# Kernel optimization log

Hardware: AMD Instinct MI355X
Metric: run time of the kernel (lower is better)

The kernel has to match this reference:

```python
import jax, jax.numpy as jnp
import numpy as np

N_NODES = 8192
N_EDGES = 262144
IN_DIM = 256
HID = 256
OUT_DIM = 64
PATH_DIM = 64
N_HEADS = 4


def setup_inputs() -> dict:
    key = jax.random.key(0)
    ks = jax.random.split(key, 16)
    s = 0.05
    x = jax.random.normal(ks[0], (N_NODES, IN_DIM), dtype=jnp.float32)
    edge_index = jax.random.randint(ks[1], (2, N_EDGES), 0, N_NODES, dtype=jnp.int32)
    return {
        "x": x,
        "edge_index": edge_index,
        # pathway encoder Linear(IN_DIM, PATH_DIM)
        "pe_w": jax.random.normal(ks[2], (IN_DIM, PATH_DIM), jnp.float32) * s,
        "pe_b": jax.random.normal(ks[3], (PATH_DIM,), jnp.float32) * s,
        # MultiheadAttention packed in-proj [3E, E] and out-proj [E, E]
        "in_proj_w": jax.random.normal(ks[4], (3 * PATH_DIM, PATH_DIM), jnp.float32) * s,
        "in_proj_b": jax.random.normal(ks[5], (3 * PATH_DIM,), jnp.float32) * s,
        "out_proj_w": jax.random.normal(ks[6], (PATH_DIM, PATH_DIM), jnp.float32) * s,
        "out_proj_b": jax.random.normal(ks[7], (PATH_DIM,), jnp.float32) * s,
        # GCN layer weights (in_dim, out_dim) + bias
        "w1": jax.random.normal(ks[8], (IN_DIM + PATH_DIM, HID), jnp.float32) * s,
        "b1": jax.random.normal(ks[9], (HID,), jnp.float32) * s,
        "w2": jax.random.normal(ks[10], (HID, HID), jnp.float32) * s,
        "b2": jax.random.normal(ks[11], (HID,), jnp.float32) * s,
        "w3": jax.random.normal(ks[12], (HID, OUT_DIM), jnp.float32) * s,
        "b3": jax.random.normal(ks[13], (OUT_DIM,), jnp.float32) * s,
    }


def mha_self(x, in_proj_w, in_proj_b, out_proj_w, out_proj_b):
    # unbatched nn.MultiheadAttention: x [N, E], Q=K=V=x
    N, E = x.shape
    dh = E // N_HEADS
    qkv = x @ in_proj_w.T + in_proj_b  # [N, 3E]
    q, k, v = jnp.split(qkv, 3, axis=-1)
    # [H, N, dh]
    q = q.reshape(N, N_HEADS, dh).transpose(1, 0, 2)
    k = k.reshape(N, N_HEADS, dh).transpose(1, 0, 2)
    v = v.reshape(N, N_HEADS, dh).transpose(1, 0, 2)
    scores = jnp.einsum('hnd,hmd->hnm', q, k) / jnp.sqrt(jnp.float32(dh))
    attn = jax.nn.softmax(scores, axis=-1)
    out = jnp.einsum('hnm,hmd->hnd', attn, v)  # [H, N, dh]
    out = out.transpose(1, 0, 2).reshape(N, E)
    return out @ out_proj_w.T + out_proj_b


def gcn_conv(h, edge_index, w, b, num_nodes):
    # PyG GCNConv: add self loops, symmetric normalization, linear, scatter-add, bias
    src = jnp.concatenate([edge_index[0], jnp.arange(num_nodes, dtype=edge_index.dtype)])
    dst = jnp.concatenate([edge_index[1], jnp.arange(num_nodes, dtype=edge_index.dtype)])
    deg = jax.ops.segment_sum(jnp.ones_like(dst, dtype=h.dtype), dst, num_segments=num_nodes)
    dinv = jnp.where(deg > 0, jax.lax.rsqrt(jnp.maximum(deg, 1e-12)), 0.0)
    hw = h @ w  # [N, out]
    norm = (dinv[src] * dinv[dst])[:, None]
    msg = hw[src] * norm
    out = jax.ops.segment_sum(msg, dst, num_segments=num_nodes)
    return out + b


def reference(x, edge_index, pe_w, pe_b, in_proj_w, in_proj_b, out_proj_w, out_proj_b,
              w1, b1, w2, b2, w3, b3):
    N = x.shape[0]
    pf = x @ pe_w + pe_b  # pathway encoder
    pa = mha_self(pf, in_proj_w, in_proj_b, out_proj_w, out_proj_b)
    h = jnp.concatenate([x, pa], axis=-1)  # [N, IN_DIM + PATH_DIM]
    h = jax.nn.relu(gcn_conv(h, edge_index, w1, b1, N))  # dropout is identity (eval)
    h = jax.nn.relu(gcn_conv(h, edge_index, w2, b2, N))
    h = gcn_conv(h, edge_index, w3, b3, N)
    return h
```

## Files before the change

kernel.cpp:

```cpp
#include <hip/hip_runtime.h>
#include <hip/hip_bf16.h>

#define N_NODES 8192
#define N_EDGES 262144
#define IN_DIM 256
#define HID 256
#define OUT_DIM 64
#define PATH_DIM 64
#define NHEADS 4
#define DH 16
#define KSPLIT 8
#define SPLIT_KEYS (N_NODES / KSPLIT)
#define NCHUNK (SPLIT_KEYS / 64)

typedef __attribute__((ext_vector_type(8))) short bf16x8;
typedef __attribute__((ext_vector_type(4))) float f32x4;

__device__ __forceinline__ ushort f2bf(float f) {
  union { float f; unsigned int u; } c;
  c.f = f;
  unsigned int u = c.u;
  u += 0x7fffu + ((u >> 16) & 1u);
  return (ushort)(u >> 16);
}

__device__ __forceinline__ float fast_exp2(float x) {
  float r;
  asm("v_exp_f32 %0, %1" : "=v"(r) : "v"(x));
  return r;
}

__device__ __forceinline__ unsigned pack_bf16(float a, float b) {
  union { __hip_bfloat162 h; unsigned u; } c;
  c.h = __float22bfloat162_rn(make_float2(a, b));
  return c.u;
}


__global__ __launch_bounds__(256) void init_graph(int* deg, int* cursor) {
  int i = blockIdx.x * 256 + threadIdx.x;
  if (i < N_NODES) { deg[i] = 1; cursor[i] = 0; }
}

__global__ __launch_bounds__(256) void count_deg(const int* __restrict__ dst,
                                                 int* __restrict__ deg) {
  int e = blockIdx.x * 256 + threadIdx.x;
  if (e < N_EDGES) atomicAdd(&deg[dst[e]], 1);
}

__global__ __launch_bounds__(256) void scan_rows(const int* __restrict__ deg,
                                                 int* __restrict__ row_off,
                                                 float* __restrict__ dinv) {
  __shared__ int part[256];
  int t = threadIdx.x;
  int base = t * 32;
  int local[32];
  int s = 0;
  #pragma unroll
  for (int i = 0; i < 32; ++i) {
    int c = deg[base + i] - 1;
    local[i] = s;
    s += c;
  }
  part[t] = s;
  __syncthreads();
  for (int d = 1; d < 256; d <<= 1) {
    int v = (t >= d) ? part[t - d] : 0;
    __syncthreads();
    part[t] += v;
    __syncthreads();
  }
  int prev = (t == 0) ? 0 : part[t - 1];
  #pragma unroll
  for (int i = 0; i < 32; ++i) {
    row_off[base + i] = prev + local[i];
    dinv[base + i] = rsqrtf((float)deg[base + i]);
  }
}

__global__ __launch_bounds__(256) void fill_csr(const int* __restrict__ src,
                                                const int* __restrict__ dst,
                                                const int* __restrict__ row_off,
                                                int* __restrict__ cursor,
                                                int* __restrict__ csr) {
  int e = blockIdx.x * 256 + threadIdx.x;
  if (e < N_EDGES) {
    int d = dst[e];
    int p = atomicAdd(&cursor[d], 1);
    csr[row_off[d] + p] = src[e];
  }
}


__global__ __launch_bounds__(256) void transpose_w(const float* __restrict__ W,
                                                   float* __restrict__ Wt,
                                                   int R, int C) {
  int i = blockIdx.x * 256 + threadIdx.x;
  if (i < R * C) {
    int r = i / C, c = i % C;
    Wt[c * R + r] = W[i];
  }
}

__global__ __launch_bounds__(256) void convert_qkv(const float* __restrict__ qkv,
                                                   ushort* __restrict__ Qbf,
                                                   ushort* __restrict__ Kbf,
                                                   ushort* __restrict__ Vtb) {
  const int tg = blockIdx.x * 256 + threadIdx.x;
  const int h = tg >> 13;
  const int n = tg & 8191;
  const float SC = 0.36067376022224085f;
  const float* base = qkv + (size_t)n * 192 + h * 16;
  ushort* qd = Qbf + ((size_t)h * 8192 + n) * 32;
  ushort* kd = Kbf + ((size_t)h * 8192 + n) * 32;
  ushort4 zz = make_ushort4(0, 0, 0, 0);
  #pragma unroll
  for (int i = 0; i < 16; i += 4) {
    float4 q4 = *reinterpret_cast<const float4*>(base + i);
    float4 k4 = *reinterpret_cast<const float4*>(base + 64 + i);
    float4 v4 = *reinterpret_cast<const float4*>(base + 128 + i);
    *reinterpret_cast<ushort4*>(qd + i) =
        make_ushort4(f2bf(q4.x * SC), f2bf(q4.y * SC), f2bf(q4.z * SC), f2bf(q4.w * SC));
    *reinterpret_cast<ushort4*>(kd + i) =
        make_ushort4(f2bf(k4.x), f2bf(k4.y), f2bf(k4.z), f2bf(k4.w));
    *reinterpret_cast<ushort4*>(qd + 16 + i) = zz;
    *reinterpret_cast<ushort4*>(kd + 16 + i) = zz;
    Vtb[((size_t)h * 16 + i + 0) * 8192 + n] = f2bf(v4.x);
    Vtb[((size_t)h * 16 + i + 1) * 8192 + n] = f2bf(v4.y);
    Vtb[((size_t)h * 16 + i + 2) * 8192 + n] = f2bf(v4.z);
    Vtb[((size_t)h * 16 + i + 3) * 8192 + n] = f2bf(v4.w);
  }
}


template <bool RELU, bool BIAS>
__global__ __launch_bounds__(256) void gemm_tile(const float* __restrict__ A1, int K1,
                                                 const float* __restrict__ A2, int K2,
                                                 const float* __restrict__ B,
                                                 const float* __restrict__ bias,
                                                 float* __restrict__ C, int N) {
  __shared__ __align__(16) float As[16][64];
  __shared__ __align__(16) float Bs[16][68];
  const int K = K1 + K2;
  const int bm = blockIdx.y * 64;
  const int bn = blockIdx.x * 64;
  const int t = threadIdx.x;
  const int tx = t & 15, ty = t >> 4;
  const int am = t >> 2;
  const int ak = (t & 3) << 2;
  const int bk = t >> 4;
  const int bn4 = (t & 15) << 2;
  float acc[4][4] = {};
  for (int k0 = 0; k0 < K; k0 += 16) {
    int kk = k0 + ak;
    int row = bm + am;
    float4 av;
    if (kk < K1)
      av = *reinterpret_cast<const float4*>(A1 + (size_t)row * K1 + kk);
    else
      av = *reinterpret_cast<const float4*>(A2 + (size_t)row * K2 + (kk - K1));
    As[ak + 0][am] = av.x;
    As[ak + 1][am] = av.y;
    As[ak + 2][am] = av.z;
    As[ak + 3][am] = av.w;
    float4 bv = *reinterpret_cast<const float4*>(B + (size_t)(k0 + bk) * N + bn + bn4);
    *reinterpret_cast<float4*>(&Bs[bk][bn4]) = bv;
    __syncthreads();
    #pragma unroll
    for (int k = 0; k < 16; ++k) {
      float4 a = *reinterpret_cast<const float4*>(&As[k][ty << 2]);
      float4 b = *reinterpret_cast<const float4*>(&Bs[k][tx << 2]);
      acc[0][0] += a.x * b.x; acc[0][1] += a.x * b.y; acc[0][2] += a.x * b.z; acc[0][3] += a.x * b.w;
      acc[1][0] += a.y * b.x; acc[1][1] += a.y * b.y; acc[1][2] += a.y * b.z; acc[1][3] += a.y * b.w;
      acc[2][0] += a.z * b.x; acc[2][1] += a.z * b.y; acc[2][2] += a.z * b.z; acc[2][3] += a.z * b.w;
      acc[3][0] += a.w * b.x; acc[3][1] += a.w * b.y; acc[3][2] += a.w * b.z; acc[3][3] += a.w * b.w;
    }
    __syncthreads();
  }
  #pragma unroll
  for (int i = 0; i < 4; ++i) {
    int row = bm + (ty << 2) + i;
    float4 o = make_float4(acc[i][0], acc[i][1], acc[i][2], acc[i][3]);
    if (BIAS) {
      float4 bv = *reinterpret_cast<const float4*>(bias + bn + (tx << 2));
      o.x += bv.x; o.y += bv.y; o.z += bv.z; o.w += bv.w;
    }
    if (RELU) {
      o.x = fmaxf(o.x, 0.f); o.y = fmaxf(o.y, 0.f);
      o.z = fmaxf(o.z, 0.f); o.w = fmaxf(o.w, 0.f);
    }
    *reinterpret_cast<float4*>(C + (size_t)row * N + bn + (tx << 2)) = o;
  }
}


__global__ __launch_bounds__(256) void attn_mfma4(const ushort* __restrict__ Qbf,
                                                  const ushort* __restrict__ Kbf,
                                                  const ushort* __restrict__ Vtb,
                                                  float* __restrict__ Opart,
                                                  float* __restrict__ Wpart) {
  const int h  = blockIdx.y;
  const int qb = blockIdx.x;
  const int kz = blockIdx.z;
  const int t  = threadIdx.x;
  const int wv = t >> 6;
  const int l  = t & 63;
  const int lg = l >> 4;
  const int lc = l & 15;

  __shared__ __align__(16) ushort Ps[64][64];
  __shared__ __align__(16) ushort Vls[2][16][64];
  __shared__ float wred[4][64];

  bf16x8 qf[4];
  {
    const ushort* qbase = Qbf + ((size_t)h * 8192 + qb * 64) * 32;
    #pragma unroll
    for (int qt = 0; qt < 4; ++qt)
      qf[qt] = *reinterpret_cast<const bf16x8*>(qbase + (qt * 16 + lc) * 32 + lg * 8);
  }

  const ushort* kbase =
      Kbf + (size_t)h * 8192 * 32 + ((size_t)kz * SPLIT_KEYS + wv * 16 + lc) * 32 + lg * 8;

  const int vrow = t >> 4;
  const int vcol8 = t & 15;
  const ushort* vsrc = Vtb + ((size_t)h * 16 + vrow) * 8192 + kz * SPLIT_KEYS + vcol8 * 4;
  const int vdst = vrow * 128 + (((vcol8 >> 1) ^ (vrow & 7)) << 4) + (vcol8 & 1) * 8;

  const int pw_off = (((wv * 2 + (lg >> 1)) ^ (lc & 7)) << 4) + (lg & 1) * 8;
  int pr_off[2], vr_off[2];
  #pragma unroll
  for (int half = 0; half < 2; ++half) {
    int g = (half * 4 + lg) ^ (lc & 7);
    pr_off[half] = (wv * 16 + lc) * 128 + g * 16;
    vr_off[half] = lc * 128 + g * 16;
  }

  char* ps_base  = (char*)&Ps[0][0];
  char* vls_base = (char*)&Vls[0][0][0];

  *reinterpret_cast<ushort4*>(vls_base + vdst) =
      *reinterpret_cast<const ushort4*>(vsrc);
  bf16x8 kf = *reinterpret_cast<const bf16x8*>(kbase);

  f32x4 oacc = {0.f, 0.f, 0.f, 0.f};
  float wsumP[4] = {0.f, 0.f, 0.f, 0.f};

  __syncthreads();

  for (int c = 0; c < NCHUNK; ++c) {
    const bool more = (c + 1 < NCHUNK);
    ushort4 vpre;
    bf16x8 kf_n;
    if (more) {
      vpre = *reinterpret_cast<const ushort4*>(vsrc + (c + 1) * 64);
      kf_n = *reinterpret_cast<const bf16x8*>(kbase + (size_t)(c + 1) * 64 * 32);
    }

    f32x4 s[4];
    #pragma unroll
    for (int qt = 0; qt < 4; ++qt) {
      f32x4 z = {0.f, 0.f, 0.f, 0.f};
      s[qt] = __builtin_amdgcn_mfma_f32_16x16x32_bf16(kf, qf[qt], z, 0, 0, 0);
    }
    kf = kf_n;

    #pragma unroll
    for (int qt = 0; qt < 4; ++qt) {
      float e0 = fast_exp2(s[qt][0]);
      float e1 = fast_exp2(s[qt][1]);
      float e2 = fast_exp2(s[qt][2]);
      float e3 = fast_exp2(s[qt][3]);
      wsumP[qt] += (e0 + e1) + (e2 + e3);
      uint2 pk;
      pk.x = pack_bf16(e0, e1);
      pk.y = pack_bf16(e2, e3);
      *reinterpret_cast<uint2*>(ps_base + (qt * 16 + lc) * 128 + pw_off) = pk;
    }

    if (more)
      *reinterpret_cast<ushort4*>(vls_base + ((c + 1) & 1) * 2048 + vdst) = vpre;

    __syncthreads();

    char* vlb = vls_base + (c & 1) * 2048;
    #pragma unroll
    for (int half = 0; half < 2; ++half) {
      bf16x8 pf = *reinterpret_cast<const bf16x8*>(ps_base + pr_off[half]);
      bf16x8 vf = *reinterpret_cast<const bf16x8*>(vlb + vr_off[half]);
      oacc = __builtin_amdgcn_mfma_f32_16x16x32_bf16(pf, vf, oacc, 0, 0, 0);
    }

    __syncthreads();
  }

  #pragma unroll
  for (int qt = 0; qt < 4; ++qt) {
    float v = wsumP[qt];
    v += __shfl_xor(v, 16);
    v += __shfl_xor(v, 32);
    wsumP[qt] = v;
  }
  if (lg == 0) {
    #pragma unroll
    for (int qt = 0; qt < 4; ++qt) wred[wv][qt * 16 + lc] = wsumP[qt];
  }
  __syncthreads();

  const size_t obase = ((size_t)(kz * NHEADS + h) * N_NODES + qb * 64);
  #pragma unroll
  for (int r = 0; r < 4; ++r) {
    const int qrow = wv * 16 + lg * 4 + r;
    Opart[(obase + qrow) * 16 + lc] = oacc[r];
  }
  if (t < 64) {
    float ws = wred[0][t] + wred[1][t] + wred[2][t] + wred[3][t];
    Wpart[obase + t] = ws;
  }
}

__global__ __launch_bounds__(256) void attn_combine(const float* __restrict__ Opart,
                                                    const float* __restrict__ Wpart,
                                                    float* __restrict__ attn_out) {
  int i = blockIdx.x * 256 + threadIdx.x;
  int dq = i & 3;
  int hn = i >> 2;
  int h = hn >> 13;
  int n = hn & 8191;
  float4 acc = make_float4(0.f, 0.f, 0.f, 0.f);
  float ws = 0.f;
  #pragma unroll
  for (int s = 0; s < KSPLIT; ++s) {
    const size_t row = ((size_t)(s * NHEADS + h) * N_NODES + n);
    float4 v = *reinterpret_cast<const float4*>(Opart + row * 16 + dq * 4);
    acc.x += v.x; acc.y += v.y; acc.z += v.z; acc.w += v.w;
    ws += Wpart[row];
  }
  float inv = 1.f / ws;
  float4 o = make_float4(acc.x * inv, acc.y * inv, acc.z * inv, acc.w * inv);
  *reinterpret_cast<float4*>(attn_out + (size_t)n * 64 + h * 16 + dq * 4) = o;
}


template <bool RELU>
__global__ __launch_bounds__(256) void aggregate2(const float* __restrict__ hw,
                                                  const int* __restrict__ csr,
                                                  const int* __restrict__ row_off,
                                                  const int* __restrict__ deg,
                                                  const float* __restrict__ dinv,
                                                  const float* __restrict__ bias,
                                                  float* __restrict__ out) {
  __shared__ __align__(16) float part[2][256];
  const int t = threadIdx.x;
  const int rw = t >> 7;
  const int wh = (t >> 6) & 1;
  const int l = t & 63;
  const int r = blockIdx.x * 2 + rw;
  const float dr = dinv[r];
  const int off = row_off[r];
  const int cnt = deg[r] - 1;
  const int c = l << 2;

  float ax, ay, az, aw;
  if (wh == 0) {
    float4 a = *reinterpret_cast<const float4*>(hw + (size_t)r * 256 + c);
    ax = dr * a.x; ay = dr * a.y; az = dr * a.z; aw = dr * a.w;
  } else {
    ax = ay = az = aw = 0.f;
  }
  for (int e = wh; e < cnt; e += 2) {
    int s = csr[off + e];
    float wsc = dinv[s];
    float4 hv = *reinterpret_cast<const float4*>(hw + (size_t)s * 256 + c);
    ax += wsc * hv.x; ay += wsc * hv.y; az += wsc * hv.z; aw += wsc * hv.w;
  }
  if (wh == 1)
    *reinterpret_cast<float4*>(&part[rw][c]) = make_float4(ax, ay, az, aw);
  __syncthreads();
  if (wh == 0) {
    float4 p = *reinterpret_cast<const float4*>(&part[rw][c]);
    float4 bv = *reinterpret_cast<const float4*>(bias + c);
    float4 o;
    o.x = dr * (ax + p.x) + bv.x;
    o.y = dr * (ay + p.y) + bv.y;
    o.z = dr * (az + p.z) + bv.z;
    o.w = dr * (aw + p.w) + bv.w;
    if (RELU) {
      o.x = fmaxf(o.x, 0.f); o.y = fmaxf(o.y, 0.f);
      o.z = fmaxf(o.z, 0.f); o.w = fmaxf(o.w, 0.f);
    }
    *reinterpret_cast<float4*>(out + (size_t)r * 256 + c) = o;
  }
}

template <bool RELU>
__global__ __launch_bounds__(256) void aggregate64(const float* __restrict__ hw,
                                                   const int* __restrict__ csr,
                                                   const int* __restrict__ row_off,
                                                   const int* __restrict__ deg,
                                                   const float* __restrict__ dinv,
                                                   const float* __restrict__ bias,
                                                   float* __restrict__ out) {
  const int w = threadIdx.x >> 6, l = threadIdx.x & 63;
  const int r = blockIdx.x * 4 + w;
  const float dr = dinv[r];
  const int off = row_off[r];
  const int cnt = deg[r] - 1;
  float a = dr * hw[(size_t)r * 64 + l];
  for (int e = 0; e < cnt; ++e) {
    int s = csr[off + e];
    a += dinv[s] * hw[(size_t)s * 64 + l];
  }
  float o = dr * a + bias[l];
  if (RELU) o = fmaxf(o, 0.f);
  out[(size_t)r * 64 + l] = o;
}


extern "C" void kernel_launch(void* const* d_in, const int* in_sizes, int n_in,
                              void* d_out, int out_size, void* d_ws, size_t ws_size,
                              hipStream_t stream) {
  const float* x          = (const float*)d_in[0];
  const int*   ei         = (const int*)d_in[1];
  const float* pe_w       = (const float*)d_in[2];
  const float* pe_b       = (const float*)d_in[3];
  const float* in_proj_w  = (const float*)d_in[4];
  const float* in_proj_b  = (const float*)d_in[5];
  const float* out_proj_w = (const float*)d_in[6];
  const float* out_proj_b = (const float*)d_in[7];
  const float* w1         = (const float*)d_in[8];
  const float* b1         = (const float*)d_in[9];
  const float* w2         = (const float*)d_in[10];
  const float* b2         = (const float*)d_in[11];
  const float* w3         = (const float*)d_in[12];
  const float* b3         = (const float*)d_in[13];

  const int* esrc = ei;
  const int* edst = ei + N_EDGES;

  char* ws = (char*)d_ws;
  size_t o = 0;
  auto take = [&](size_t n) {
    char* p = ws + o;
    o += (n + 255) & ~(size_t)255;
    return p;
  };
  float* pf       = (float*)take((size_t)N_NODES * PATH_DIM * 4);
  float* qkv      = (float*)take((size_t)N_NODES * 3 * PATH_DIM * 4);
  float* attn_out = (float*)take((size_t)N_NODES * PATH_DIM * 4);
  float* pa       = (float*)take((size_t)N_NODES * PATH_DIM * 4);
  float* hw       = (float*)take((size_t)N_NODES * HID * 4);
  float* h1       = (float*)take((size_t)N_NODES * HID * 4);
  float* h2       = (float*)take((size_t)N_NODES * HID * 4);
  float* Wt_in    = (float*)take((size_t)3 * PATH_DIM * PATH_DIM * 4);
  float* Wt_out   = (float*)take((size_t)PATH_DIM * PATH_DIM * 4);
  float* dinv     = (float*)take((size_t)N_NODES * 4);
  int*   deg      = (int*)take((size_t)N_NODES * 4);
  int*   cursor   = (int*)take((size_t)N_NODES * 4);
  int*   row_off  = (int*)take((size_t)N_NODES * 4);
  int*   csr      = (int*)take((size_t)N_EDGES * 4);

  ushort* Qbf = (ushort*)h2;
  ushort* Kbf = Qbf + (size_t)NHEADS * N_NODES * 32;
  ushort* Vtb = Kbf + (size_t)NHEADS * N_NODES * 32;
  float* Opart = hw;
  float* Wpart = pa;

  init_graph<<<N_NODES / 256, 256, 0, stream>>>(deg, cursor);
  count_deg<<<N_EDGES / 256, 256, 0, stream>>>(edst, deg);
  scan_rows<<<1, 256, 0, stream>>>(deg, row_off, dinv);
  fill_csr<<<N_EDGES / 256, 256, 0, stream>>>(esrc, edst, row_off, cursor, csr);

  transpose_w<<<(192 * 64 + 255) / 256, 256, 0, stream>>>(in_proj_w, Wt_in, 192, 64);
  transpose_w<<<(64 * 64 + 255) / 256, 256, 0, stream>>>(out_proj_w, Wt_out, 64, 64);

  gemm_tile<false, true><<<dim3(1, 128), 256, 0, stream>>>(x, IN_DIM, nullptr, 0, pe_w, pe_b, pf, PATH_DIM);
  gemm_tile<false, true><<<dim3(3, 128), 256, 0, stream>>>(pf, PATH_DIM, nullptr, 0, Wt_in, in_proj_b, qkv, 3 * PATH_DIM);

  convert_qkv<<<(N_NODES * NHEADS) / 256, 256, 0, stream>>>(qkv, Qbf, Kbf, Vtb);
  attn_mfma4<<<dim3(128, 4, KSPLIT), 256, 0, stream>>>(Qbf, Kbf, Vtb, Opart, Wpart);
  attn_combine<<<(NHEADS * N_NODES * 4) / 256, 256, 0, stream>>>(Opart, Wpart, attn_out);

  gemm_tile<false, true><<<dim3(1, 128), 256, 0, stream>>>(attn_out, PATH_DIM, nullptr, 0, Wt_out, out_proj_b, pa, PATH_DIM);

  gemm_tile<false, false><<<dim3(4, 128), 256, 0, stream>>>(x, IN_DIM, pa, PATH_DIM, w1, nullptr, hw, HID);
  aggregate2<true><<<N_NODES / 2, 256, 0, stream>>>(hw, csr, row_off, deg, dinv, b1, h1);
  gemm_tile<false, false><<<dim3(4, 128), 256, 0, stream>>>(h1, HID, nullptr, 0, w2, nullptr, hw, HID);
  aggregate2<true><<<N_NODES / 2, 256, 0, stream>>>(hw, csr, row_off, deg, dinv, b2, h2);
  gemm_tile<false, false><<<dim3(1, 128), 256, 0, stream>>>(h2, HID, nullptr, 0, w3, nullptr, hw, OUT_DIM);
  aggregate64<false><<<N_NODES / 4, 256, 0, stream>>>(hw, csr, row_off, deg, dinv, b3, (float*)d_out);
}
```

Before: 296.7 us.

## Keep attention probabilities in registers and feed PV MFMA directly

The attention kernel no longer stages P and V through shared memory with two barriers per chunk. Each wave now uses the QK^T MFMA output layout directly as the A operand of a 16x16x16 bf16 MFMA and loads V from global memory per wave. Each wave keeps its own partial output for all 64 queries, and the four waves are reduced through LDS once at the end. This removes the per-iteration LDS traffic and syncs, at the cost of more accumulator registers and a final cross-wave reduction.

Result: no change. 296.9 us, median of 4 (+0.1%).

```diff
diff --git a/kernel.cpp b/kernel.cpp
--- a/kernel.cpp
+++ b/kernel.cpp
@@ -11,9 +11,10 @@
 #define DH 16
 #define KSPLIT 8
 #define SPLIT_KEYS (N_NODES / KSPLIT)
-#define NCHUNK (SPLIT_KEYS / 64)
+#define NITER (SPLIT_KEYS / 64)
 
 typedef __attribute__((ext_vector_type(8))) short bf16x8;
+typedef __attribute__((ext_vector_type(4))) short bf16x4;
 typedef __attribute__((ext_vector_type(4))) float f32x4;
 
 __device__ __forceinline__ ushort f2bf(float f) {
@@ -35,6 +36,19 @@
   c.h = __float22bfloat162_rn(make_float2(a, b));
   return c.u;
 }
+
+#if __has_builtin(__builtin_amdgcn_mfma_f32_16x16x16bf16_1k)
+__device__ __forceinline__ f32x4 mfma16(bf16x4 a, bf16x4 b, f32x4 c) {
+  return __builtin_amdgcn_mfma_f32_16x16x16bf16_1k(a, b, c, 0, 0, 0);
+}
+#else
+__device__ __forceinline__ f32x4 mfma16(bf16x4 a, bf16x4 b, f32x4 c) {
+  f32x4 d;
+  asm volatile("v_mfma_f32_16x16x16_bf16 %0, %1, %2, %3\n\ts_nop 7\n\ts_nop 3"
+               : "=v"(d) : "v"(a), "v"(b), "v"(c));
+  return d;
+}
+#endif
 
 
 __global__ __launch_bounds__(256) void init_graph(int* deg, int* cursor) {
@@ -194,7 +208,7 @@
 }
 
 
-__global__ __launch_bounds__(256) void attn_mfma4(const ushort* __restrict__ Qbf,
+__global__ __launch_bounds__(256) void attn_mfma5(const ushort* __restrict__ Qbf,
                                                   const ushort* __restrict__ Kbf,
                                                   const ushort* __restrict__ Vtb,
                                                   float* __restrict__ Opart,
@@ -208,9 +222,8 @@
   const int lg = l >> 4;
   const int lc = l & 15;
 
-  __shared__ __align__(16) ushort Ps[64][64];
-  __shared__ __align__(16) ushort Vls[2][16][64];
-  __shared__ float wred[4][64];
+  __shared__ float red_o[3][64][17];
+  __shared__ float red_w[3][64];
 
   bf16x8 qf[4];
   {
@@ -220,42 +233,24 @@
       qf[qt] = *reinterpret_cast<const bf16x8*>(qbase + (qt * 16 + lc) * 32 + lg * 8);
   }
 
-  const ushort* kbase =
-      Kbf + (size_t)h * 8192 * 32 + ((size_t)kz * SPLIT_KEYS + wv * 16 + lc) * 32 + lg * 8;
-
-  const int vrow = t >> 4;
-  const int vcol8 = t & 15;
-  const ushort* vsrc = Vtb + ((size_t)h * 16 + vrow) * 8192 + kz * SPLIT_KEYS + vcol8 * 4;
-  const int vdst = vrow * 128 + (((vcol8 >> 1) ^ (vrow & 7)) << 4) + (vcol8 & 1) * 8;
-
-  const int pw_off = (((wv * 2 + (lg >> 1)) ^ (lc & 7)) << 4) + (lg & 1) * 8;
-  int pr_off[2], vr_off[2];
-  #pragma unroll
-  for (int half = 0; half < 2; ++half) {
-    int g = (half * 4 + lg) ^ (lc & 7);
-    pr_off[half] = (wv * 16 + lc) * 128 + g * 16;
-    vr_off[half] = lc * 128 + g * 16;
-  }
-
-  char* ps_base  = (char*)&Ps[0][0];
-  char* vls_base = (char*)&Vls[0][0][0];
-
-  *reinterpret_cast<ushort4*>(vls_base + vdst) =
-      *reinterpret_cast<const ushort4*>(vsrc);
-  bf16x8 kf = *reinterpret_cast<const bf16x8*>(kbase);
-
-  f32x4 oacc = {0.f, 0.f, 0.f, 0.f};
-  float wsumP[4] = {0.f, 0.f, 0.f, 0.f};
-
-  __syncthreads();
-
-  for (int c = 0; c < NCHUNK; ++c) {
-    const bool more = (c + 1 < NCHUNK);
-    ushort4 vpre;
+  const ushort* kptr =
+      Kbf + ((size_t)h * 8192 + kz * SPLIT_KEYS + wv * 16 + lc) * 32 + lg * 8;
+  const ushort* vptr =
+      Vtb + ((size_t)h * 16 + lc) * 8192 + kz * SPLIT_KEYS + wv * 16 + lg * 4;
+
+  f32x4 oacc[4] = {{0.f, 0.f, 0.f, 0.f}, {0.f, 0.f, 0.f, 0.f},
+                   {0.f, 0.f, 0.f, 0.f}, {0.f, 0.f, 0.f, 0.f}};
+  float wsum[4] = {0.f, 0.f, 0.f, 0.f};
+
+  bf16x8 kf = *reinterpret_cast<const bf16x8*>(kptr);
+  bf16x4 vf = *reinterpret_cast<const bf16x4*>(vptr);
+
+  for (int c = 0; c < NITER; ++c) {
     bf16x8 kf_n;
-    if (more) {
-      vpre = *reinterpret_cast<const ushort4*>(vsrc + (c + 1) * 64);
-      kf_n = *reinterpret_cast<const bf16x8*>(kbase + (size_t)(c + 1) * 64 * 32);
+    bf16x4 vf_n;
+    if (c + 1 < NITER) {
+      kf_n = *reinterpret_cast<const bf16x8*>(kptr + (size_t)(c + 1) * 64 * 32);
+      vf_n = *reinterpret_cast<const bf16x4*>(vptr + (size_t)(c + 1) * 64);
     }
 
     f32x4 s[4];
@@ -264,7 +259,6 @@
       f32x4 z = {0.f, 0.f, 0.f, 0.f};
       s[qt] = __builtin_amdgcn_mfma_f32_16x16x32_bf16(kf, qf[qt], z, 0, 0, 0);
     }
-    kf = kf_n;
 
     #pragma unroll
     for (int qt = 0; qt < 4; ++qt) {
@@ -272,51 +266,54 @@
       float e1 = fast_exp2(s[qt][1]);
       float e2 = fast_exp2(s[qt][2]);
       float e3 = fast_exp2(s[qt][3]);
-      wsumP[qt] += (e0 + e1) + (e2 + e3);
+      wsum[qt] += (e0 + e1) + (e2 + e3);
       uint2 pk;
       pk.x = pack_bf16(e0, e1);
       pk.y = pack_bf16(e2, e3);
-      *reinterpret_cast<uint2*>(ps_base + (qt * 16 + lc) * 128 + pw_off) = pk;
-    }
-
-    if (more)
-      *reinterpret_cast<ushort4*>(vls_base + ((c + 1) & 1) * 2048 + vdst) = vpre;
-
-    __syncthreads();
-
-    char* vlb = vls_base + (c & 1) * 2048;
-    #pragma unroll
-    for (int half = 0; half < 2; ++half) {
-      bf16x8 pf = *reinterpret_cast<const bf16x8*>(ps_base + pr_off[half]);
-      bf16x8 vf = *reinterpret_cast<const bf16x8*>(vlb + vr_off[half]);
-      oacc = __builtin_amdgcn_mfma_f32_16x16x32_bf16(pf, vf, oacc, 0, 0, 0);
-    }
-
-    __syncthreads();
+      bf16x4 pf;
+      pf[0] = (short)(pk.x & 0xffff); pf[1] = (short)(pk.x >> 16);
+      pf[2] = (short)(pk.y & 0xffff); pf[3] = (short)(pk.y >> 16);
+      oacc[qt] = mfma16(pf, vf, oacc[qt]);
+    }
+
+    kf = kf_n;
+    vf = vf_n;
   }
 
   #pragma unroll
   for (int qt = 0; qt < 4; ++qt) {
-    float v = wsumP[qt];
+    float v = wsum[qt];
     v += __shfl_xor(v, 16);
     v += __shfl_xor(v, 32);
-    wsumP[qt] = v;
-  }
-  if (lg == 0) {
-    #pragma unroll
-    for (int qt = 0; qt < 4; ++qt) wred[wv][qt * 16 + lc] = wsumP[qt];
+    wsum[qt] = v;
+  }
+
+  if (wv > 0) {
+    #pragma unroll
+    for (int qt = 0; qt < 4; ++qt) {
+      #pragma unroll
+      for (int r = 0; r < 4; ++r)
+        red_o[wv - 1][qt * 16 + lg * 4 + r][lc] = oacc[qt][r];
+      if (lg == 0) red_w[wv - 1][qt * 16 + lc] = wsum[qt];
+    }
   }
   __syncthreads();
 
-  const size_t obase = ((size_t)(kz * NHEADS + h) * N_NODES + qb * 64);
-  #pragma unroll
-  for (int r = 0; r < 4; ++r) {
-    const int qrow = wv * 16 + lg * 4 + r;
-    Opart[(obase + qrow) * 16 + lc] = oacc[r];
-  }
-  if (t < 64) {
-    float ws = wred[0][t] + wred[1][t] + wred[2][t] + wred[3][t];
-    Wpart[obase + t] = ws;
+  if (wv == 0) {
+    const size_t obase = ((size_t)(kz * NHEADS + h) * N_NODES + qb * 64);
+    #pragma unroll
+    for (int qt = 0; qt < 4; ++qt) {
+      #pragma unroll
+      for (int r = 0; r < 4; ++r) {
+        const int q = qt * 16 + lg * 4 + r;
+        float o = oacc[qt][r] + red_o[0][q][lc] + red_o[1][q][lc] + red_o[2][q][lc];
+        Opart[(obase + q) * 16 + lc] = o;
+      }
+      if (lg == 0) {
+        const int q = qt * 16 + lc;
+        Wpart[obase + q] = wsum[qt] + red_w[0][q] + red_w[1][q] + red_w[2][q];
+      }
+    }
   }
 }
 
@@ -479,7 +476,7 @@
   gemm_tile<false, true><<<dim3(3, 128), 256, 0, stream>>>(pf, PATH_DIM, nullptr, 0, Wt_in, in_proj_b, qkv, 3 * PATH_DIM);
 
   convert_qkv<<<(N_NODES * NHEADS) / 256, 256, 0, stream>>>(qkv, Qbf, Kbf, Vtb);
-  attn_mfma4<<<dim3(128, 4, KSPLIT), 256, 0, stream>>>(Qbf, Kbf, Vtb, Opart, Wpart);
+  attn_mfma5<<<dim3(128, 4, KSPLIT), 256, 0, stream>>>(Qbf, Kbf, Vtb, Opart, Wpart);
   attn_combine<<<(NHEADS * N_NODES * 4) / 256, 256, 0, stream>>>(Opart, Wpart, attn_out);
 
   gemm_tile<false, true><<<dim3(1, 128), 256, 0, stream>>>(attn_out, PATH_DIM, nullptr, 0, Wt_out, out_proj_b, pa, PATH_DIM);
```
